# Optimization experiments

Hardware: AMD Instinct MI355X
Metric: run time of the kernel (lower is better)

The kernel has to match this reference:

```python
import jax, jax.numpy as jnp
import numpy as np

V = 27578   # super-model vertex count (self.shape)
NJ = 24     # joints
NB = 10     # shape PCA coeffs
NP = (NJ - 1) * 9  # 207 pose-blend features
K = 24000   # kept vertices (to_keep)
B = 32
# standard SMPL kinematic tree: PARENTS[i] is the parent joint of joint i (i>=1)
PARENTS = np.array([0, 0, 0, 0, 1, 2, 3, 4, 5, 6, 7, 8, 9, 9, 9, 12, 13, 14, 16, 17, 18, 19, 20, 21], dtype=np.int32)


def setup_inputs() -> dict:
    key = jax.random.key(0)
    ks = jax.random.split(key, 8)
    pose = jax.random.normal(ks[0], (B, NJ, 3), dtype=jnp.float32) * 0.4
    betas = jax.random.normal(ks[1], (B, NB + 1), dtype=jnp.float32)  # last entry = gender flag
    J_regressor = jax.random.uniform(ks[2], (2, NJ, V), dtype=jnp.float32)
    J_regressor = J_regressor / jnp.sum(J_regressor, axis=-1, keepdims=True)
    v_template = jax.random.normal(ks[3], (2, V, 3), dtype=jnp.float32)
    shapedirs = jax.random.normal(ks[4], (2, V, 3, NB), dtype=jnp.float32) * 0.03
    posedirs = jax.random.normal(ks[5], (2, V, 3, NP), dtype=jnp.float32) * 0.01
    weights_all = jax.random.uniform(ks[6], (2, V, NJ), dtype=jnp.float32)
    weights_all = weights_all / jnp.sum(weights_all, axis=-1, keepdims=True)
    to_keep = jnp.sort(jax.random.randint(ks[7], (K,), 0, V, dtype=jnp.int32))
    return {"pose": pose, "betas": betas, "J_regressor": J_regressor,
            "v_template": v_template, "shapedirs": shapedirs, "posedirs": posedirs,
            "weights_all": weights_all, "to_keep": to_keep}


def rodrigues(r):
    """Axis-angle [N,3] -> rotation matrices [N,3,3] (Rodrigues formula)."""
    eps = jnp.float32(np.finfo(np.float32).eps)
    theta = jnp.maximum(jnp.linalg.norm(r, axis=-1, keepdims=True), eps)  # [N,1]
    rh = r / theta
    z = jnp.zeros_like(rh[:, 0])
    m = jnp.stack([z, -rh[:, 2], rh[:, 1],
                   rh[:, 2], z, -rh[:, 0],
                   -rh[:, 1], rh[:, 0], z], axis=1).reshape(-1, 3, 3)
    t = theta[:, :, None]  # [N,1,1]
    I = jnp.eye(3, dtype=r.dtype)
    return I + m * jnp.sin(t) + jnp.matmul(m, m) * (1.0 - jnp.cos(t))


def reference(pose, betas, J_regressor, v_template, shapedirs, posedirs, weights_all, to_keep):
    b = betas.shape[0]
    dt = pose.dtype
    g = betas[:, -1] > 0.5  # gender: True -> male (index 1)
    sel = lambda f, m: jnp.where(g[:, None, None], m, f)

    # shape blendshapes for both genders, select per sample
    vs_f = jnp.einsum('bs,vcs->bvc', betas[:, :NB], shapedirs[0]) + v_template[0]
    vs_m = jnp.einsum('bs,vcs->bvc', betas[:, :NB], shapedirs[1]) + v_template[1]

    J_f = jnp.einsum('jv,bvc->bjc', J_regressor[0], vs_f)
    J_m = jnp.einsum('jv,bvc->bjc', J_regressor[1], vs_m)
    J = sel(J_f, J_m)  # [b,24,3]

    # Rodrigues per joint
    R = rodrigues(pose.reshape(-1, 3)).reshape(b, NJ, 3, 3)

    # pose blendshapes
    lrot = (R[:, 1:] - jnp.eye(3, dtype=dt)).reshape(b, NP)  # [b,207]
    off_f = jnp.einsum('bp,vcp->bvc', lrot, posedirs[0])
    off_m = jnp.einsum('bp,vcp->bvc', lrot, posedirs[1])
    v_posed = sel(vs_f, vs_m) + sel(off_f, off_m)  # [b,V,3]

    # local joint transforms [b,24,4,4]
    J_rel = jnp.concatenate([J[:, :1], J[:, 1:] - J[:, PARENTS[1:]]], axis=1)
    A = jnp.concatenate([R, J_rel[..., None]], axis=-1)  # [b,24,3,4]
    bottom = jnp.broadcast_to(jnp.array([0., 0., 0., 1.], dtype=dt), (b, NJ, 1, 4))
    A = jnp.concatenate([A, bottom], axis=2)

    # kinematic chain (sequential 24-joint tree)
    Gs = [A[:, 0]]
    for i in range(1, NJ):
        Gs.append(jnp.matmul(Gs[int(PARENTS[i])], A[:, i]))
    G = jnp.stack(Gs, axis=1)  # [b,24,4,4]

    # subtract rest-pose joint contribution: results = G - pack(G @ [J;0])
    Jh0 = jnp.concatenate([J, jnp.zeros((b, NJ, 1), dtype=dt)], axis=-1)
    corr = jnp.einsum('bjpq,bjq->bjp', G, Jh0)
    results = G.at[:, :, :, 3].add(-corr)

    Jh1 = jnp.concatenate([J, jnp.ones((b, NJ, 1), dtype=dt)], axis=-1)
    joints = jnp.einsum('bjpq,bjq->bjp', results, Jh1)[:, :, :3]

    # linear blend skinning with gender-matched weights
    w = jnp.where(g[:, None, None], weights_all[1][None], weights_all[0][None])  # [b,V,24]
    T = jnp.einsum('bjpq,bvj->bvpq', results, w)  # [b,V,4,4]
    vh = jnp.concatenate([v_posed, jnp.ones((b, V, 1), dtype=dt)], axis=-1)
    v = jnp.einsum('bvpq,bvq->bvp', T, vh)[:, :, :3]

    root = joints[:, :1]
    result = (v - root)[:, to_keep, :]  # [b,K,3]
    return result
```

## Files before the change

kernel.cpp:

```cpp
#include <hip/hip_runtime.h>
#include <hip/hip_bf16.h>
#include <cstdint>
#include <cstddef>

#define V      27578
#define NJ     24
#define KK     24000
#define NT2    1724
#define NCHUNK 25
#define VCHUNK 1104

#define LPD    0
#define LA     12288
#define LRB    16000
#define LVP    24192
#define LT     26368
#define LWA    36608
#define LTM2   37120
#define LROOT2 37216
#define LPERM2 37312
#define LCNT2  37344
#define LKB    37348
#define LDSW   37364

#define WS_JS   0
#define WS_LA   39600
#define WS_RB   43312
#define WS_ROOT 51824
#define WS_PERM 51920
#define WS_CNT  51952
#define WS_KB   51956

typedef short short8 __attribute__((ext_vector_type(8)));
typedef float f32x4 __attribute__((ext_vector_type(4)));

union S8U4 { unsigned u[4]; uint4 u4; short8 s; };

__device__ __forceinline__ unsigned pk2(float a, float b) {
    __hip_bfloat162 h = __float22bfloat162_rn(float2{a, b});
    union { __hip_bfloat162 h; unsigned u; } cv; cv.h = h;
    return cv.u;
}

__constant__ int d_par[24] = {0,0,0,0,1,2,3,4,5,6,7,8,9,9,9,12,13,14,16,17,18,19,20,21};

__global__ __launch_bounds__(256) void k_js(const float* __restrict__ jreg,
                                            const float* __restrict__ vtmpl,
                                            const float* __restrict__ sdirs,
                                            float* __restrict__ ws) {
    const int chunk = blockIdx.x, jg = blockIdx.y, g = blockIdx.z;
    const int tid = threadIdx.x;
    float acc[4][33];
#pragma unroll
    for (int a = 0; a < 4; ++a)
#pragma unroll
        for (int o = 0; o < 33; ++o) acc[a][o] = 0.f;

    const int v0 = chunk * VCHUNK;
    const int v1 = (v0 + VCHUNK < V) ? v0 + VCHUNK : V;
    const float* jr0 = jreg + (size_t)g * NJ * V;
    const float* sd  = sdirs + (size_t)g * V * 30;
    const float* tm  = vtmpl + (size_t)g * V * 3;

    for (int v = v0 + tid; v < v1; v += 256) {
        float jv[4];
#pragma unroll
        for (int a = 0; a < 4; ++a) jv[a] = jr0[(size_t)(jg*4 + a) * V + v];
        float b[33];
        const float* sdv = sd + (size_t)v * 30;
#pragma unroll
        for (int o = 0; o < 30; o += 2) {
            float2 q = *(const float2*)(sdv + o);
            b[o] = q.x; b[o+1] = q.y;
        }
        b[30] = tm[(size_t)v*3 + 0];
        b[31] = tm[(size_t)v*3 + 1];
        b[32] = tm[(size_t)v*3 + 2];
#pragma unroll
        for (int a = 0; a < 4; ++a)
#pragma unroll
            for (int o = 0; o < 33; ++o) acc[a][o] += jv[a] * b[o];
    }

#pragma unroll
    for (int a = 0; a < 4; ++a)
#pragma unroll
        for (int o = 0; o < 33; ++o) {
            float x = acc[a][o];
#pragma unroll
            for (int s = 32; s >= 1; s >>= 1) x += __shfl_xor(x, s, 64);
            acc[a][o] = x;
        }

    __shared__ float red[4][132];
    const int wvi = tid >> 6, ln = tid & 63;
    if (ln == 0) {
#pragma unroll
        for (int a = 0; a < 4; ++a)
#pragma unroll
            for (int o = 0; o < 33; ++o) red[wvi][a*33 + o] = acc[a][o];
    }
    __syncthreads();
    if (tid < 132) {
        float s = red[0][tid] + red[1][tid] + red[2][tid] + red[3][tid];
        int a = tid / 33, o = tid % 33;
        int j = jg * 4 + a;
        ws[(size_t)((g*NJ + j)*33 + o) * NCHUNK + chunk] = s;
    }
}

__global__ __launch_bounds__(256) void k_joint(const float* __restrict__ pose,
                                               const float* __restrict__ betas,
                                               const int*   __restrict__ to_keep,
                                               float* __restrict__ ws) {
    const int bid = (int)blockIdx.x;
    const int t = threadIdx.x;
    int* wsI = (int*)ws;
    unsigned* wsU = (unsigned*)ws;

    if (bid >= 32) {
        int idx = (bid - 32) * 256 + t;
        if (idx <= NT2) {
            int target = idx * 16;
            int lo = 0, hi = KK;
            while (lo < hi) { int m = (lo + hi) >> 1; if (to_keep[m] < target) lo = m + 1; else hi = m; }
            wsI[WS_KB + idx] = lo;
        }
        return;
    }

    __shared__ float gflag[32];
    __shared__ int   permJ[33];
    __shared__ float jsJ[792];
    __shared__ float Jloc[96];
    __shared__ float AJ[288];
    __shared__ float GS[288];

    if (t < 32) gflag[t] = betas[t*11 + 10];
    __syncthreads();
    if (t < 32) {
        bool male = gflag[t] > 0.5f;
        unsigned gm = (unsigned)__ballot(male);
        int cnt0 = 32 - __popc(gm);
        unsigned below = (1u << t) - 1u;
        int slot = male ? (cnt0 + __popc(gm & below)) : __popc((~gm) & below);
        permJ[slot] = t;
        if (t == 0) permJ[32] = cnt0;
    }
    __syncthreads();

    const int slot = bid;
    const int b = permJ[slot];
    const int gi = (gflag[b] > 0.5f) ? 1 : 0;

    if (bid == 0) {
        if (t < 32) wsI[WS_PERM + t] = permJ[t];
        if (t == 0) wsI[WS_CNT] = permJ[32];
    }

    for (int o = t; o < 792; o += 256) {
        const float* p = ws + WS_JS + (size_t)(gi*792 + o) * NCHUNK;
        float s = 0.f;
#pragma unroll
        for (int c = 0; c < NCHUNK; ++c) s += p[c];
        jsJ[o] = s;
    }
    __syncthreads();

    if (t < 72) {
        int j = t / 3, c = t - 3*j;
        const float* jsb = jsJ + j*33;
        float s = jsb[30 + c];
#pragma unroll
        for (int q = 0; q < 10; ++q) s += jsb[c*10 + q] * betas[b*11 + q];
        Jloc[j*4 + c] = s;
    }
    __syncthreads();

    if (t < 24) {
        const float* pp = pose + (size_t)(b*24 + t) * 3;
        float rx = pp[0], ry = pp[1], rz = pp[2];
        float th = fmaxf(sqrtf(rx*rx + ry*ry + rz*rz), 1.1920929e-07f);
        float inv = 1.0f / th;
        float ux = rx*inv, uy = ry*inv, uz = rz*inv;
        float st = sinf(th), ct = cosf(th), oc = 1.0f - ct;
        float* A = AJ + t*12;
        A[0] = ct + oc*ux*ux;    A[1] = oc*ux*uy - st*uz; A[2]  = oc*ux*uz + st*uy;
        A[4] = oc*ux*uy + st*uz; A[5] = ct + oc*uy*uy;    A[6]  = oc*uy*uz - st*ux;
        A[8] = oc*ux*uz - st*uy; A[9] = oc*uy*uz + st*ux; A[10] = ct + oc*uz*uz;
        int par = d_par[t];
#pragma unroll
        for (int r = 0; r < 3; ++r)
            A[r*4 + 3] = Jloc[t*4 + r] - (t > 0 ? Jloc[par*4 + r] : 0.f);
    }
    __syncthreads();

    if (t < 116) {
        float f[2];
#pragma unroll
        for (int h = 0; h < 2; ++h) {
            int k = 2*t + h;
            float val = 0.f;
            if (k < 207) {
                int j = k / 9 + 1, rc = k - 9*(j-1);
                int r = rc / 3, c = rc - 3*r;
                val = AJ[j*12 + r*4 + c] - (r == c ? 1.f : 0.f);
            } else if (k >= 208 && k < 218) {
                val = betas[b*11 + (k - 208)];
            }
            f[h] = val;
        }
        wsU[WS_LA + slot*116 + t] = pk2(f[0], f[1]);
    }

    if (t < 12) {
        constexpr int kPar[24] = {0,0,0,0,1,2,3,4,5,6,7,8,9,9,9,12,13,14,16,17,18,19,20,21};
        const int r = t >> 2, c = t & 3;
        float Greg[24];
        Greg[0] = AJ[t];
#pragma unroll
        for (int j = 1; j < 24; ++j) {
            const int par = kPar[j];
            float a0 = AJ[j*12 + 0 + c];
            float a1 = AJ[j*12 + 4 + c];
            float a2 = AJ[j*12 + 8 + c];
            float g0 = __shfl(Greg[par], r*4 + 0, 64);
            float g1 = __shfl(Greg[par], r*4 + 1, 64);
            float g2 = __shfl(Greg[par], r*4 + 2, 64);
            float g3 = __shfl(Greg[par], r*4 + 3, 64);
            Greg[j] = g0*a0 + g1*a1 + g2*a2 + (c == 3 ? g3 : 0.f);
        }
#pragma unroll
        for (int j = 0; j < 24; ++j) {
            float t0 = __shfl(Greg[j], r*4 + 0, 64);
            float t1 = __shfl(Greg[j], r*4 + 1, 64);
            float t2 = __shfl(Greg[j], r*4 + 2, 64);
            float corr = t0*Jloc[j*4 + 0] + t1*Jloc[j*4 + 1] + t2*Jloc[j*4 + 2];
            if (c == 3) Greg[j] -= corr;
            GS[j*12 + t] = Greg[j];
        }
    }
    __syncthreads();

    {
        int kg = t >> 6, rem = t & 63, n = rem >> 2, wq = rem & 3;
        int j0 = kg*8 + 2*wq;
        float f0 = (j0 < 24 && n < 12) ? GS[j0*12 + n] : 0.f;
        float f1 = (j0 + 1 < 24 && n < 12) ? GS[(j0+1)*12 + n] : 0.f;
        wsU[WS_RB + slot*256 + t] = pk2(f0, f1);
    }
    if (t < 3) {
        float s = GS[t*4 + 3];
#pragma unroll
        for (int q = 0; q < 3; ++q) s += GS[t*4 + q] * Jloc[q];
        ws[WS_ROOT + slot*3 + t] = s;
    }
}

__global__ __launch_bounds__(1024) void k_pose(const float* __restrict__ posedirs,
                                               const float* __restrict__ sdirs,
                                               const float* __restrict__ vtmpl,
                                               const float* __restrict__ wall,
                                               const int*   __restrict__ to_keep,
                                               const float* __restrict__ ws,
                                               float* __restrict__ out) {
    extern __shared__ float L[];
    unsigned* Lu = (unsigned*)L;
    int* Li = (int*)L;
    const unsigned* wsU = (const unsigned*)ws;
    const int* wsI = (const int*)ws;
    const int t = threadIdx.x;
    const int l = t & 63, wv = t >> 6;
    const int lm = l & 15, lg = l >> 4;
    const int bid = (int)blockIdx.x;

    int pdoff[5], pdladr[5];
    bool pdok[5], pdq3[5];
#pragma unroll
    for (int n = 0; n < 5; ++n) {
        int e = t + 1024*n;
        bool ok = e < 4992;
        pdok[n] = ok;
        int e2 = ok ? e : 0;
        int row = e2 / 52, k4 = (e2 - 52*row) * 4;
        int g = row / 48, rr = row - 48*g;
        pdoff[n] = g*(V*621) + rr*207 + k4;
        int kw = k4 >> 1;
        pdladr[n] = LPD + row*128 + (kw ^ ((row & 7) << 2));
        pdq3[n] = (k4 == 204);
    }
    int sdoff = 0, sdladr = 0;
    if (t < 480) {
        int w = 2*t;
        int g = w / 480, w2 = w - 480*g;
        int row = w2 / 10, j = (w2 - 10*row) >> 1;
        int rowg = g*48 + row;
        sdoff = g*(V*30) + w2;
        sdladr = LPD + rowg*128 + ((104 + j) ^ ((rowg & 7) << 2));
    }
    int tmoff = 0;
    if (t < 48)  { int w = 2*t; int g = w/48;  tmoff = g*(V*3) + (w - 48*g); }
    int woff = 0, wladr = 0;
    if (t < 384) {
        int g = t/192, i = t - 192*g;
        int v = i/12, wi = i - 12*v;
        int kgrp = wi >> 2, wq = wi & 3;
        int j0 = kgrp*8 + 2*wq;
        woff = g*(V*24) + v*24 + j0;
        wladr = LWA + g*256 + kgrp*64 + v*4 + wq;
    }

    float4 pdreg[5]; float2 sdreg = {0,0}, tmreg = {0,0}, wreg = {0,0};

    const int PDLIM = 2*V*621 - 4;
    const int SDLIM = 2*V*30 - 2;
    const int TMLIM = 2*V*3 - 2;
    const int WLIM  = 2*V*24 - 2;

    auto issue_loads = [&](int itm) {
        const int vb = itm * 16;
#pragma unroll
        for (int n = 0; n < 5; ++n) {
            int a = vb*621 + pdoff[n];
            if (a > PDLIM) a = PDLIM;
            pdreg[n].x = posedirs[a];
            pdreg[n].y = posedirs[a+1];
            pdreg[n].z = posedirs[a+2];
            pdreg[n].w = pdq3[n] ? 0.f : posedirs[a+3];
        }
        if (t < 480) { int a = vb*30 + sdoff; if (a > SDLIM) a = SDLIM; sdreg = *(const float2*)(sdirs + a); }
        if (t < 48)  { int a = vb*3  + tmoff; if (a > TMLIM) a = TMLIM; tmreg = *(const float2*)(vtmpl + a); }
        if (t < 384) { int a = vb*24 + woff;  if (a > WLIM)  a = WLIM;  wreg  = *(const float2*)(wall  + a); }
    };

    auto write_stage = [&]() {
#pragma unroll
        for (int n = 0; n < 5; ++n)
            if (pdok[n]) {
                uint2 v;
                v.x = pk2(pdreg[n].x, pdreg[n].y);
                v.y = pk2(pdreg[n].z, pdreg[n].w);
                *(uint2*)&Lu[pdladr[n]] = v;
            }
        if (t < 480) Lu[sdladr] = pk2(sdreg.x, sdreg.y);
        if (t < 48)  { L[LTM2 + 2*t] = tmreg.x; L[LTM2 + 2*t + 1] = tmreg.y; }
        if (t < 384) Lu[wladr] = pk2(wreg.x, wreg.y);
    };

    issue_loads(bid);

    {
        for (int i = t; i < 928; i += 1024)
            *(uint4*)&Lu[LA + 4*i] = *(const uint4*)&wsU[WS_LA + 4*i];
        for (int i = t; i < 2048; i += 1024)
            *(uint4*)&Lu[LRB + 4*i] = *(const uint4*)&wsU[WS_RB + 4*i];
        if (t < 96)  L[LROOT2 + t] = ws[WS_ROOT + t];
        if (t < 32)  Li[LPERM2 + t] = wsI[WS_PERM + t];
        if (t == 0)  Li[LCNT2] = wsI[WS_CNT];
        if (t < 8) {
            int idx = bid + 256*t;
            int kst = KK, ken = KK;
            if (idx < NT2) { kst = wsI[WS_KB + idx]; ken = wsI[WS_KB + idx + 1]; }
            Li[LKB + t] = kst; Li[LKB + 8 + t] = ken;
        }
        if (t < 128) Lu[LWA + (t >> 6)*256 + 192 + (t & 63)] = 0;
        if (t < 288) {
            int row = t / 3, j2 = 109 + (t - 3*(t/3));
            Lu[LPD + row*128 + (j2 ^ ((row & 7) << 2))] = 0;
        }
        __syncthreads();
    }

    const int cnt0v = Li[LCNT2];
    const int cnt1 = 32 - cnt0v;
    const int m0 = (cnt0v + 15) >> 4, m1 = (cnt1 + 15) >> 4;
    const int ntA = 3*m0, ntasks = 3*(m0 + m1);

    int rb0 = -1, nt0 = 0, sb0 = 0, ct0 = 0, gi0 = 0;
    if (wv < ntasks) {
        int gi = (wv >= ntA) ? 1 : 0; int tt = gi ? wv - ntA : wv;
        int mt = tt / 3; nt0 = tt - 3*mt;
        sb0 = gi ? cnt0v : 0; ct0 = gi ? cnt1 : cnt0v;
        rb0 = sb0 + mt*16; gi0 = gi;
    }

    const int bs = t >> 5, kl0 = t & 31;
    const int borig = Li[LPERM2 + bs];
    const float rt0 = L[LROOT2 + bs*3 + 0];
    const float rt1 = L[LROOT2 + bs*3 + 1];
    const float rt2 = L[LROOT2 + bs*3 + 2];
    const int s4 = (lm & 7) << 2;

    write_stage();
    __syncthreads();

    int li = 0;
    for (int item = bid; item < NT2; item += 256, ++li) {
        const bool more = (item + 256 < NT2);
        if (more) issue_loads(item + 256);

        f32x4 acc0 = {0,0,0,0};
        if (rb0 >= 0) {
            const unsigned* ap = Lu + LA + (rb0 + lm)*116 + (lg << 2);
            const unsigned* bp = Lu + LPD + (gi0*48 + nt0*16 + lm)*128;
#pragma unroll
            for (int kk = 0; kk < 7; ++kk) {
                S8U4 a; a.u4 = *(const uint4*)(ap + kk*16);
                S8U4 bb; bb.u4 = *(const uint4*)(bp + ((kk*16 + (lg << 2)) ^ s4));
                acc0 = __builtin_amdgcn_mfma_f32_16x16x32_bf16(a.s, bb.s, acc0, 0, 0, 0);
            }
        }

        if (rb0 >= 0) {
            int n = nt0*16 + lm;
            int vd = n / 3, cd = n - 3*vd;
            float tmv = L[LTM2 + gi0*48 + n];
#pragma unroll
            for (int r = 0; r < 4; ++r) {
                int slot = rb0 + (lg << 2) + r;
                if ((unsigned)(slot - sb0) < (unsigned)ct0)
                    L[LVP + slot*68 + vd*4 + cd] = acc0[r] + tmv;
            }
        }

#pragma unroll
        for (int q = 0; q < 2; ++q) {
            int s = wv*2 + q;
            int gsl = (s >= cnt0v) ? 1 : 0;
            S8U4 a; a.u4 = *(const uint4*)(Lu + LWA + gsl*256 + lg*64 + lm*4);
            S8U4 b; b.u4 = *(const uint4*)(Lu + LRB + s*256 + lg*64 + lm*4);
            f32x4 acT = {0,0,0,0};
            acT = __builtin_amdgcn_mfma_f32_16x16x32_bf16(a.s, b.s, acT, 0, 0, 0);
#pragma unroll
            for (int r = 0; r < 4; ++r)
                L[LT + s*320 + (lg*4 + r)*20 + lm] = acT[r];
        }
        __syncthreads();

        const int kst = Li[LKB + li], ken = Li[LKB + 8 + li];
        const int v0w = item * 16;
        for (int k = kst + kl0; k < ken; k += 32) {
            const int vr = to_keep[k] - v0w;
            const float4 vp = *(const float4*)&L[LVP + bs*68 + vr*4];
            const float4 t0 = *(const float4*)&L[LT + bs*320 + vr*20];
            const float4 t1 = *(const float4*)&L[LT + bs*320 + vr*20 + 4];
            const float4 t2 = *(const float4*)&L[LT + bs*320 + vr*20 + 8];
            const size_t ob = ((size_t)borig*KK + (size_t)k)*3;
            out[ob]   = t0.x*vp.x + t0.y*vp.y + t0.z*vp.z + t0.w - rt0;
            out[ob+1] = t1.x*vp.x + t1.y*vp.y + t1.z*vp.z + t1.w - rt1;
            out[ob+2] = t2.x*vp.x + t2.y*vp.y + t2.z*vp.z + t2.w - rt2;
        }
        if (more) write_stage();
        __syncthreads();
    }
}

extern "C" void kernel_launch(void* const* d_in, const int* in_sizes, int n_in,
                              void* d_out, int out_size, void* d_ws, size_t ws_size,
                              hipStream_t stream) {
    const float* pose     = (const float*)d_in[0];
    const float* betas    = (const float*)d_in[1];
    const float* jreg     = (const float*)d_in[2];
    const float* vtmpl    = (const float*)d_in[3];
    const float* sdirs    = (const float*)d_in[4];
    const float* posedirs = (const float*)d_in[5];
    const float* wall     = (const float*)d_in[6];
    const int*   to_keep  = (const int*)d_in[7];
    float* ws  = (float*)d_ws;
    float* out = (float*)d_out;

    hipFuncSetAttribute((const void*)k_pose,
                        hipFuncAttributeMaxDynamicSharedMemorySize,
                        LDSW * 4);

    hipLaunchKernelGGL(k_js,    dim3(NCHUNK, 6, 2), dim3(256), 0, stream, jreg, vtmpl, sdirs, ws);
    hipLaunchKernelGGL(k_joint, dim3(40),           dim3(256), 0, stream, pose, betas, to_keep, ws);
    hipLaunchKernelGGL(k_pose,  dim3(256),          dim3(1024), LDSW * 4, stream,
                       posedirs, sdirs, vtmpl, wall, to_keep, ws, out);
}
```

Before: 81.93 us.

## Stage shapedirs through LDS in k_js and use lighter barriers in k_pose

k_js now loads each 256-vertex tile of shapedirs and the template cooperatively into shared memory with coalesced loads, instead of each thread doing strided float2 reads. k_pose gets a waves-per-EU hint on its launch bounds, and two __syncthreads calls become an inline-asm barrier that waits only on LDS counters, not on outstanding global stores. The LDS staging adds two block barriers per tile to k_js. The custom barrier depends on global stores not needing to be ordered across that point.

Measured after the change: 104.9 us. 28.0% more time.

```diff
diff --git a/kernel.cpp b/kernel.cpp
--- a/kernel.cpp
+++ b/kernel.cpp
@@ -42,6 +42,11 @@
     return cv.u;
 }
 
+#define BAR_LGKM() do { \
+    asm volatile("s_waitcnt lgkmcnt(0)\n\ts_barrier" ::: "memory"); \
+    __builtin_amdgcn_sched_barrier(0); \
+} while (0)
+
 __constant__ int d_par[24] = {0,0,0,0,1,2,3,4,5,6,7,8,9,9,9,12,13,14,16,17,18,19,20,21};
 
 __global__ __launch_bounds__(256) void k_js(const float* __restrict__ jreg,
@@ -50,6 +55,10 @@
                                             float* __restrict__ ws) {
     const int chunk = blockIdx.x, jg = blockIdx.y, g = blockIdx.z;
     const int tid = threadIdx.x;
+    __shared__ float sdt[256 * 30];
+    __shared__ float tmt[256 * 3];
+    __shared__ float red[4][132];
+
     float acc[4][33];
 #pragma unroll
     for (int a = 0; a < 4; ++a)
@@ -62,24 +71,30 @@
     const float* sd  = sdirs + (size_t)g * V * 30;
     const float* tm  = vtmpl + (size_t)g * V * 3;
 
-    for (int v = v0 + tid; v < v1; v += 256) {
-        float jv[4];
-#pragma unroll
-        for (int a = 0; a < 4; ++a) jv[a] = jr0[(size_t)(jg*4 + a) * V + v];
-        float b[33];
-        const float* sdv = sd + (size_t)v * 30;
-#pragma unroll
-        for (int o = 0; o < 30; o += 2) {
-            float2 q = *(const float2*)(sdv + o);
-            b[o] = q.x; b[o+1] = q.y;
-        }
-        b[30] = tm[(size_t)v*3 + 0];
-        b[31] = tm[(size_t)v*3 + 1];
-        b[32] = tm[(size_t)v*3 + 2];
-#pragma unroll
-        for (int a = 0; a < 4; ++a)
-#pragma unroll
-            for (int o = 0; o < 33; ++o) acc[a][o] += jv[a] * b[o];
+    for (int vt = v0; vt < v1; vt += 256) {
+        const int cnt = (v1 - vt < 256) ? (v1 - vt) : 256;
+        const float* sb = sd + (size_t)vt * 30;
+        const float* tb = tm + (size_t)vt * 3;
+        const int nsd = cnt * 30, ntm = cnt * 3;
+        __syncthreads();
+        for (int i = tid; i < nsd; i += 256) sdt[i] = sb[i];
+        for (int i = tid; i < ntm; i += 256) tmt[i] = tb[i];
+        __syncthreads();
+        if (tid < cnt) {
+            const int v = vt + tid;
+            float jv[4];
+#pragma unroll
+            for (int a = 0; a < 4; ++a) jv[a] = jr0[(size_t)(jg*4 + a) * V + v];
+            const float* bb = sdt + tid * 30;
+            const float* tt = tmt + tid * 3;
+#pragma unroll
+            for (int a = 0; a < 4; ++a) {
+#pragma unroll
+                for (int o = 0; o < 30; ++o) acc[a][o] += jv[a] * bb[o];
+#pragma unroll
+                for (int c = 0; c < 3; ++c) acc[a][30 + c] += jv[a] * tt[c];
+            }
+        }
     }
 
 #pragma unroll
@@ -92,7 +107,6 @@
             acc[a][o] = x;
         }
 
-    __shared__ float red[4][132];
     const int wvi = tid >> 6, ln = tid & 63;
     if (ln == 0) {
 #pragma unroll
@@ -257,13 +271,13 @@
     }
 }
 
-__global__ __launch_bounds__(1024) void k_pose(const float* __restrict__ posedirs,
-                                               const float* __restrict__ sdirs,
-                                               const float* __restrict__ vtmpl,
-                                               const float* __restrict__ wall,
-                                               const int*   __restrict__ to_keep,
-                                               const float* __restrict__ ws,
-                                               float* __restrict__ out) {
+__global__ __launch_bounds__(1024, 4) void k_pose(const float* __restrict__ posedirs,
+                                                  const float* __restrict__ sdirs,
+                                                  const float* __restrict__ vtmpl,
+                                                  const float* __restrict__ wall,
+                                                  const int*   __restrict__ to_keep,
+                                                  const float* __restrict__ ws,
+                                                  float* __restrict__ out) {
     extern __shared__ float L[];
     unsigned* Lu = (unsigned*)L;
     int* Li = (int*)L;
@@ -435,7 +449,7 @@
             for (int r = 0; r < 4; ++r)
                 L[LT + s*320 + (lg*4 + r)*20 + lm] = acT[r];
         }
-        __syncthreads();
+        BAR_LGKM();
 
         const int kst = Li[LKB + li], ken = Li[LKB + 8 + li];
         const int v0w = item * 16;
@@ -451,7 +465,7 @@
             out[ob+2] = t2.x*vp.x + t2.y*vp.y + t2.z*vp.z + t2.w - rt2;
         }
         if (more) write_stage();
-        __syncthreads();
+        BAR_LGKM();
     }
 }
 
```
